# Optimization experiments

Hardware: AMD Instinct MI355X
Metric: run time of the kernel (lower is better)

The kernel has to match this reference:

```python
import jax, jax.numpy as jnp
import numpy as np

B, N, H, NH, M = 4, 8192, 1024, 16, 64
D = H // NH  # head_dim = 64
SCALE = D ** -0.5


def setup_inputs() -> dict:
    key = jax.random.key(0)
    ks = jax.random.split(key, 10)
    inp = {
        'x': jax.random.normal(ks[0], (B, N, H), jnp.float32),
        'c': jax.random.normal(ks[1], (B, H), jnp.float32),
        'w_kv': jax.random.normal(ks[2], (H, 2 * H), jnp.float32) * (H ** -0.5),
        'b_kv': jnp.zeros((2 * H,), jnp.float32),
        'w_temp': jax.random.normal(ks[3], (H, NH), jnp.float32) * (H ** -0.5),
        'b_temp': jnp.zeros((NH,), jnp.float32),
        'xq': jax.random.normal(ks[4], (NH, M, D), jnp.float32) * (D ** -0.5),
        'qkv_proj': jax.random.normal(ks[5], (NH, D, 3 * D), jnp.float32) * 0.02,
        'w_out': jax.random.normal(ks[6], (H, H), jnp.float32) * (H ** -0.5),
        'b_out': jnp.zeros((H,), jnp.float32),
    }
    return inp


def reference(x, c, w_kv, b_kv, w_temp, b_temp, xq, qkv_proj, w_out, b_out):
    b, n, h = x.shape
    # kv slice projections -> [b, h, n, d]
    kv = x @ w_kv + b_kv
    xk, xv = jnp.split(kv, 2, axis=-1)
    xk = xk.reshape(b, n, NH, D).transpose(0, 2, 1, 3)
    xv = xv.reshape(b, n, NH, D).transpose(0, 2, 1, 3)
    # per-token learned temperature: [b, n, heads] -> [b, heads, 1, n]
    temperature = 0.5 + jax.nn.softplus(x @ w_temp + b_temp)
    temperature = temperature.transpose(0, 2, 1)[:, :, None, :]
    # slice scores and softmax over SLICE (query) dim m
    slice_scores = jnp.einsum('hmd,bhnd->bhmn', xq, xk)
    slice_weights = jax.nn.softmax(slice_scores / temperature, axis=-2)
    slice_norm = slice_weights.sum(axis=-1)  # [b, h, m]
    slice_token = jnp.einsum('bhmn,bhnd->bhmd', slice_weights, xv)
    slice_token = slice_token / (slice_norm[..., None] + 1e-5)
    # tiny intra-slice 'attention' (faithfully elementwise, softmax over d)
    qkv = jnp.einsum('bhmd,hde->bhme', slice_token, qkv_proj)
    q_t, k_t, v_t = jnp.split(qkv, 3, axis=-1)
    dots = q_t * k_t * SCALE          # einsum 'bhqd,bhdq->bhqd' == elementwise
    attn = jax.nn.softmax(dots, axis=-1)
    out_slice_token = attn * v_t       # einsum 'bhqd,bhqd->bhqd' == elementwise
    # scatter back to tokens via slice_weights
    out_x = jnp.einsum('bhmd,bhmn->bhnd', out_slice_token, slice_weights)
    out_x = out_x.transpose(0, 2, 1, 3).reshape(b, n, h)
    return out_x @ w_out + b_out
```

## Files before the change

kernel.cpp:

```cpp
#include <hip/hip_runtime.h>
#include <hip/hip_bf16.h>


#define NTOK 32768
#define HH   1024
#define NHD  16
#define DD   64

typedef short short8 __attribute__((ext_vector_type(8)));
typedef float f32x4 __attribute__((ext_vector_type(4)));

#define AS1 __attribute__((address_space(1)))
#define AS3 __attribute__((address_space(3)))

__device__ __forceinline__ void glds16(const void* g, void* l) {
  __builtin_amdgcn_global_load_lds((const AS1 void*)g, (AS3 void*)l, 16, 0, 0);
}

__device__ __forceinline__ void split1(float v, __hip_bfloat16& h, __hip_bfloat16& l) {
  h = __float2bfloat16(v);
  l = __float2bfloat16(v - __bfloat162float(h));
}


__global__ __launch_bounds__(256) void k_acat_t(const float* __restrict__ w_kv,
                                                const float* __restrict__ xq,
                                                __hip_bfloat16* __restrict__ wbth,
                                                __hip_bfloat16* __restrict__ wbtl) {
  int hd = blockIdx.x >> 3, kt = blockIdx.x & 7, k0 = kt * 128;
  __shared__ float xqs[64 * 65];
  __shared__ float wks[128 * 65];
  int t = threadIdx.x;
  for (int j = 0; j < 16; ++j) {
    int idx = t + 256 * j; int m = idx >> 6, d = idx & 63;
    xqs[m * 65 + d] = xq[hd * 4096 + idx];
  }
  for (int j = 0; j < 32; ++j) {
    int idx = t + 256 * j; int r = idx >> 6, c = idx & 63;
    wks[r * 65 + c] = w_kv[(size_t)(k0 + r) * 2048 + hd * 64 + c];
  }
  __syncthreads();
  int m = t & 63, kg = t >> 6;
  __hip_bfloat16 hbuf[32], lbuf[32];
  for (int i = 0; i < 32; ++i) {
    int k = kg * 32 + i;
    float s = 0.f;
    #pragma unroll 8
    for (int d = 0; d < 64; ++d) s = fmaf(wks[k * 65 + d], xqs[m * 65 + d], s);
    split1(s, hbuf[i], lbuf[i]);
  }
  size_t o = (size_t)(hd * 64 + m) * 1024 + k0 + kg * 32;
  for (int i = 0; i < 32; i += 8) {
    *(uint4*)&wbth[o + i] = *(uint4*)&hbuf[i];
    *(uint4*)&wbtl[o + i] = *(uint4*)&lbuf[i];
  }
}

__global__ __launch_bounds__(256) void k_tsplit(const float* __restrict__ src, int ld,
                                                __hip_bfloat16* __restrict__ dh,
                                                __hip_bfloat16* __restrict__ dl) {
  __shared__ float tile[64 * 65];
  int br = blockIdx.y * 64, bc = blockIdx.x * 64;
  int t = threadIdx.x;
  for (int j = 0; j < 16; ++j) {
    int idx = t + 256 * j; int r = idx >> 6, c = idx & 63;
    tile[r * 65 + c] = src[(size_t)(br + r) * ld + bc + c];
  }
  __syncthreads();
  for (int j = 0; j < 16; ++j) {
    int idx = t + 256 * j; int c = idx >> 6, r = idx & 63;
    float v = tile[r * 65 + c];
    __hip_bfloat16 hv, lv; split1(v, hv, lv);
    size_t o = (size_t)(bc + c) * 1024 + br + r;
    dh[o] = hv; dl[o] = lv;
  }
}

__global__ void k_split(const float* __restrict__ src, __hip_bfloat16* __restrict__ hi,
                        __hip_bfloat16* __restrict__ lo) {
  size_t base = ((size_t)blockIdx.x * 256 + threadIdx.x) * 8;
  float4 v0 = *(const float4*)&src[base];
  float4 v1 = *(const float4*)&src[base + 4];
  float vv[8] = {v0.x, v0.y, v0.z, v0.w, v1.x, v1.y, v1.z, v1.w};
  __hip_bfloat16 h8[8], l8[8];
  #pragma unroll
  for (int i = 0; i < 8; ++i) split1(vv[i], h8[i], l8[i]);
  *(uint4*)&hi[base] = *(uint4*)h8;
  *(uint4*)&lo[base] = *(uint4*)l8;
}

__global__ __launch_bounds__(512, 2) void k_mfma8(
    const __hip_bfloat16* __restrict__ Ah, const __hip_bfloat16* __restrict__ Al,
    const __hip_bfloat16* __restrict__ Bh, const __hip_bfloat16* __restrict__ Bl,
    const float* __restrict__ bias, float* __restrict__ C, int ldc) {
  __shared__ __align__(16) char lds[131072];
  const int t = threadIdx.x;
  const int w = t >> 6, lane = t & 63;

  const int gx = gridDim.x;
  const int nwg = gx * gridDim.y;
  const int bid = blockIdx.y * gx + blockIdx.x;
  const int swzb = (bid & 7) * (nwg >> 3) + (bid >> 3);
  const int n0 = (swzb % gx) * 256;
  const int m0 = (swzb / gx) * 256;

  const int wr = w >> 2, wc = w & 3;
  const int fm = lane & 15, kq = lane >> 4;

  int offA[8], offB[4];
  #pragma unroll
  for (int i = 0; i < 8; ++i) {
    int row = wr * 128 + i * 16 + fm;
    offA[i] = (row >> 1) * 128 + ((((row & 1) << 2) | kq) ^ ((row >> 1) & 7)) * 16;
  }
  #pragma unroll
  for (int j = 0; j < 4; ++j) {
    int row = wc * 64 + j * 16 + fm;
    offB[j] = (row >> 1) * 128 + ((((row & 1) << 2) | kq) ^ ((row >> 1) & 7)) * 16;
  }

  const int sp = lane >> 3, su = (lane & 7) ^ sp;
  const int srow = 2 * sp + (su >> 2);
  const int scol = (su & 3) * 8;
  const int aO0 = (m0 + w * 16 + srow) * 1024 + scol;
  const int aO1 = aO0 + 128 * 1024;
  const int bO0 = (n0 + w * 16 + srow) * 1024 + scol;
  const int bO1 = bO0 + 128 * 1024;
  const int ldst = w * 1024 + lane * 16;

  f32x4 acc[8][4];
  #pragma unroll
  for (int i = 0; i < 8; ++i)
    #pragma unroll
    for (int j = 0; j < 4; ++j) acc[i][j] = (f32x4){0.f, 0.f, 0.f, 0.f};

  auto stage = [&](int ts) {
    int koff = (ts >> 1) * 32;
    char* buf = &lds[(ts & 3) * 32768];
    const __hip_bfloat16* As = (ts & 1) ? Al : Ah;
    const __hip_bfloat16* Bs = (ts & 1) ? Bl : Bh;
    glds16(As + aO0 + koff, buf + ldst);
    glds16(As + aO1 + koff, buf + 8192 + ldst);
    glds16(Bs + bO0 + koff, buf + 16384 + ldst);
    glds16(Bs + bO1 + koff, buf + 24576 + ldst);
  };

  stage(0); stage(1); stage(2);
  asm volatile("s_waitcnt vmcnt(8)" ::: "memory");
  __builtin_amdgcn_s_barrier();
  __builtin_amdgcn_sched_barrier(0);

  short8 ah[8], bh[4], xb[4];
  for (int k = 0; k < 32; ++k) {
    const int v0 = 2 * k, v1 = v0 + 1;
    const char* rb0 = &lds[(v0 & 3) * 32768];
    const char* rb1 = &lds[(v1 & 3) * 32768];

    int ts0 = v0 + 3; if (ts0 > 63) ts0 = 63;
    stage(ts0);
    #pragma unroll
    for (int i = 0; i < 8; ++i) ah[i] = *(const short8*)(rb0 + offA[i]);
    #pragma unroll
    for (int j = 0; j < 4; ++j) bh[j] = *(const short8*)(rb0 + 16384 + offB[j]);
    __builtin_amdgcn_s_setprio(1);
    #pragma unroll
    for (int i = 0; i < 8; ++i)
      #pragma unroll
      for (int j = 0; j < 4; ++j)
        acc[i][j] = __builtin_amdgcn_mfma_f32_16x16x32_bf16(ah[i], bh[j], acc[i][j], 0, 0, 0);
    __builtin_amdgcn_s_setprio(0);
    asm volatile("s_waitcnt vmcnt(8)" ::: "memory");
    __builtin_amdgcn_s_barrier();
    __builtin_amdgcn_sched_barrier(0);

    int ts1 = v1 + 3; if (ts1 > 63) ts1 = 63;
    stage(ts1);
    #pragma unroll
    for (int j = 0; j < 4; ++j) xb[j] = *(const short8*)(rb1 + 16384 + offB[j]);
    __builtin_amdgcn_s_setprio(1);
    #pragma unroll
    for (int i = 0; i < 8; ++i)
      #pragma unroll
      for (int j = 0; j < 4; ++j)
        acc[i][j] = __builtin_amdgcn_mfma_f32_16x16x32_bf16(ah[i], xb[j], acc[i][j], 0, 0, 0);
    __builtin_amdgcn_s_setprio(0);
    #pragma unroll
    for (int i = 0; i < 8; ++i) ah[i] = *(const short8*)(rb1 + offA[i]);
    __builtin_amdgcn_s_setprio(1);
    #pragma unroll
    for (int i = 0; i < 8; ++i)
      #pragma unroll
      for (int j = 0; j < 4; ++j)
        acc[i][j] = __builtin_amdgcn_mfma_f32_16x16x32_bf16(ah[i], bh[j], acc[i][j], 0, 0, 0);
    __builtin_amdgcn_s_setprio(0);
    asm volatile("s_waitcnt vmcnt(8)" ::: "memory");
    __builtin_amdgcn_s_barrier();
    __builtin_amdgcn_sched_barrier(0);
  }

  asm volatile("s_waitcnt vmcnt(0)" ::: "memory");
  __builtin_amdgcn_sched_barrier(0);

  const int cm = (lane >> 4) * 4, cn = lane & 15;
  #pragma unroll
  for (int j = 0; j < 4; ++j) {
    int col = n0 + wc * 64 + j * 16 + cn;
    float bbv = bias[col];
    #pragma unroll
    for (int i = 0; i < 8; ++i) {
      int row = m0 + wr * 128 + i * 16 + cm;
      f32x4 v = acc[i][j];
      #pragma unroll
      for (int r = 0; r < 4; ++r)
        C[(size_t)(row + r) * ldc + col] = v[r] + bbv;
    }
  }
}

__global__ __launch_bounds__(256) void k_acat(const float* __restrict__ w_kv,
                                              const float* __restrict__ xq,
                                              float* __restrict__ wbig) {
  int h = blockIdx.x >> 3, kt = blockIdx.x & 7, k0 = kt * 128;
  __shared__ float xqs[64 * 68];
  __shared__ float wks[128 * 68];
  int t = threadIdx.x;
  for (int j = 0; j < 16; ++j) {
    int idx = t + 256 * j; int m = idx >> 6, d = idx & 63;
    xqs[m * 68 + d] = xq[h * 4096 + idx];
  }
  for (int j = 0; j < 32; ++j) {
    int idx = t + 256 * j; int r = idx >> 6, c = idx & 63;
    wks[r * 68 + c] = w_kv[(k0 + r) * 2048 + h * 64 + c];
  }
  __syncthreads();
  int k = t >> 1, half = t & 1;
  float out[32];
  for (int mi = 0; mi < 32; ++mi) {
    int m = half * 32 + mi;
    float s = 0.f;
    #pragma unroll 8
    for (int d = 0; d < 64; ++d) s = fmaf(wks[k * 68 + d], xqs[m * 68 + d], s);
    out[mi] = s;
  }
  float* dst = &wbig[(k0 + k) * 2048 + h * 64 + half * 32];
  for (int mi = 0; mi < 32; mi += 4)
    *(float4*)(dst + mi) = make_float4(out[mi], out[mi + 1], out[mi + 2], out[mi + 3]);
}

__global__ void k_copyv(const float* __restrict__ w_kv, float* __restrict__ wbig) {
  int idx4 = blockIdx.x * 256 + threadIdx.x;
  int k = idx4 >> 8, j4 = idx4 & 255;
  int off = k * 2048 + 1024 + j4 * 4;
  *(float4*)(wbig + off) = *(const float4*)(w_kv + off);
}

__global__ void k_bias1(const float* __restrict__ xq, const float* __restrict__ b_kv,
                        float* __restrict__ bias1) {
  int j = blockIdx.x * 256 + threadIdx.x;
  if (j < 1024) {
    int h = j >> 6, m = j & 63;
    float s = 0.f;
    for (int d = 0; d < 64; ++d) s = fmaf(xq[h * 4096 + m * 64 + d], b_kv[h * 64 + d], s);
    bias1[j] = s;
  } else {
    bias1[j] = b_kv[j];
  }
}

__global__ __launch_bounds__(256) void k_temp(const float* __restrict__ x,
                                              const float* __restrict__ w_temp,
                                              const float* __restrict__ b_temp,
                                              float* __restrict__ T) {
  __shared__ float xs[16 * 1028];
  int t = threadIdx.x;
  int bn0 = blockIdx.x * 16;
  for (int j = 0; j < 16; ++j) {
    int idx4 = t + 256 * j; int row = idx4 >> 8, c4 = (idx4 & 255) * 4;
    *(float4*)&xs[row * 1028 + c4] = *(const float4*)&x[(bn0 + row) * 1024 + c4];
  }
  __syncthreads();
  int tok = t >> 4, j = t & 15;
  float z = b_temp[j];
  for (int k = 0; k < 1024; ++k) z = fmaf(xs[tok * 1028 + k], w_temp[k * 16 + j], z);
  float sp = fmaxf(z, 0.f) + log1pf(expf(-fabsf(z)));
  T[(bn0 + tok) * 16 + j] = 0.5f + sp;
}

__global__ __launch_bounds__(256) void k_gemm(const float* __restrict__ A, int lda,
                                              const float* __restrict__ Bm, int ldb,
                                              const float* __restrict__ bias,
                                              float* __restrict__ C, int ldc, int K) {
  __shared__ float As[8 * 132];
  __shared__ float Bs[8 * 132];
  int t = threadIdx.x;
  int m0 = blockIdx.y * 128, n0 = blockIdx.x * 128;
  int ar = t >> 1, ac = (t & 1) * 4;
  int bk = t >> 5, bc = (t & 31) * 4;
  const float* Ag = A + (size_t)(m0 + ar) * lda + ac;
  const float* Bg = Bm + (size_t)bk * ldb + n0 + bc;
  int tx = t & 15, ty = t >> 4;
  float acc[8][8] = {};
  float4 a4 = *(const float4*)Ag;
  float4 b4 = *(const float4*)Bg;
  for (int kt = 0; kt < K; kt += 8) {
    __syncthreads();
    As[(ac + 0) * 132 + ar] = a4.x;
    As[(ac + 1) * 132 + ar] = a4.y;
    As[(ac + 2) * 132 + ar] = a4.z;
    As[(ac + 3) * 132 + ar] = a4.w;
    *(float4*)&Bs[bk * 132 + bc] = b4;
    __syncthreads();
    if (kt + 8 < K) {
      a4 = *(const float4*)(Ag + kt + 8);
      b4 = *(const float4*)(Bg + (size_t)(kt + 8) * ldb);
    }
    #pragma unroll
    for (int k = 0; k < 8; ++k) {
      float av[8], bv[8];
      *(float4*)&av[0] = *(float4*)&As[k * 132 + ty * 8];
      *(float4*)&av[4] = *(float4*)&As[k * 132 + ty * 8 + 4];
      *(float4*)&bv[0] = *(float4*)&Bs[k * 132 + tx * 4];
      *(float4*)&bv[4] = *(float4*)&Bs[k * 132 + 64 + tx * 4];
      #pragma unroll
      for (int i = 0; i < 8; ++i)
        #pragma unroll
        for (int j = 0; j < 8; ++j) acc[i][j] = fmaf(av[i], bv[j], acc[i][j]);
    }
  }
  float4 bb0 = *(const float4*)&bias[n0 + tx * 4];
  float4 bb1 = *(const float4*)&bias[n0 + 64 + tx * 4];
  #pragma unroll
  for (int i = 0; i < 8; ++i) {
    float* crow = C + (size_t)(m0 + ty * 8 + i) * ldc + n0;
    float4 o0 = make_float4(acc[i][0] + bb0.x, acc[i][1] + bb0.y,
                            acc[i][2] + bb0.z, acc[i][3] + bb0.w);
    float4 o1 = make_float4(acc[i][4] + bb1.x, acc[i][5] + bb1.y,
                            acc[i][6] + bb1.z, acc[i][7] + bb1.w);
    *(float4*)&crow[tx * 4] = o0;
    *(float4*)&crow[64 + tx * 4] = o1;
  }
}

__global__ __launch_bounds__(256) void k_smax(float* __restrict__ S, const float* __restrict__ T,
                                              float* __restrict__ token, float* __restrict__ norm) {
  int pair = blockIdx.x >> 3, chunk = blockIdx.x & 7;
  int b = pair >> 4, h = pair & 15;
  __shared__ float sm[128 * 68];
  __shared__ float xv[128 * 68];
  int t = threadIdx.x;
  int m = t >> 2, dg = t & 3;
  float acc[16] = {};
  float nacc = 0.f;
  for (int s = 0; s < 8; ++s) {
    int bn0 = b * 8192 + chunk * 1024 + s * 128;
    for (int jj = 0; jj < 8; ++jj) {
      int idx4 = t + 256 * jj; int row = idx4 >> 4, c4 = (idx4 & 15) * 4;
      int g = (bn0 + row) * 2048 + h * 64 + c4;
      *(float4*)&sm[row * 68 + c4] = *(const float4*)&S[g];
      *(float4*)&xv[row * 68 + c4] = *(const float4*)&S[g + 1024];
    }
    __syncthreads();
    if (t < 128) {
      float tt = T[(bn0 + t) * 16 + h];
      float inv = 1.f / tt;
      float* row = &sm[t * 68];
      float mx = -1e30f;
      for (int mm = 0; mm < 64; ++mm) mx = fmaxf(mx, row[mm]);
      float sum = 0.f;
      for (int mm = 0; mm < 64; ++mm) { float e = expf((row[mm] - mx) * inv); row[mm] = e; sum += e; }
      float sinv = 1.f / sum;
      for (int mm = 0; mm < 64; ++mm) row[mm] *= sinv;
    }
    __syncthreads();
    for (int jj = 0; jj < 8; ++jj) {
      int idx4 = t + 256 * jj; int row = idx4 >> 4, c4 = (idx4 & 15) * 4;
      int g = (bn0 + row) * 2048 + h * 64 + c4;
      *(float4*)&S[g] = *(const float4*)&sm[row * 68 + c4];
    }
    for (int n = 0; n < 128; ++n) {
      float w = sm[n * 68 + m];
      if (dg == 0) nacc += w;
      const float* xr = &xv[n * 68 + dg * 16];
      #pragma unroll
      for (int q = 0; q < 4; ++q) {
        float4 v = *(const float4*)&xr[q * 4];
        acc[q * 4 + 0] = fmaf(w, v.x, acc[q * 4 + 0]);
        acc[q * 4 + 1] = fmaf(w, v.y, acc[q * 4 + 1]);
        acc[q * 4 + 2] = fmaf(w, v.z, acc[q * 4 + 2]);
        acc[q * 4 + 3] = fmaf(w, v.w, acc[q * 4 + 3]);
      }
    }
    __syncthreads();
  }
  int tb = pair * 4096 + m * 64 + dg * 16;
  for (int q = 0; q < 16; ++q) atomicAdd(&token[tb + q], acc[q]);
  if (dg == 0) atomicAdd(&norm[pair * 64 + m], nacc);
}

__global__ __launch_bounds__(256) void k_stagec(const float* __restrict__ token,
                                                const float* __restrict__ norm,
                                                const float* __restrict__ proj,
                                                float* __restrict__ ost) {
  int pair = blockIdx.x; int h = pair & 15;
  __shared__ float st[64 * 68];
  __shared__ float qk[64 * 196];
  int t = threadIdx.x;
  for (int j = 0; j < 16; ++j) {
    int idx = t + 256 * j; int m = idx >> 6, d = idx & 63;
    st[m * 68 + d] = token[pair * 4096 + idx] / (norm[pair * 64 + m] + 1e-5f);
  }
  __syncthreads();
  for (int idx = t; idx < 64 * 192; idx += 256) {
    int m = idx / 192, e = idx % 192;
    float s = 0.f;
    const float* pr = &proj[h * 12288 + e];
    const float* sr = &st[m * 68];
    for (int d = 0; d < 64; ++d) s = fmaf(sr[d], pr[d * 192], s);
    qk[m * 196 + e] = s;
  }
  __syncthreads();
  if (t < 64) {
    const float* q = &qk[t * 196];
    float dots[64];
    float mx = -1e30f;
    for (int d = 0; d < 64; ++d) { dots[d] = q[d] * q[64 + d] * 0.125f; mx = fmaxf(mx, dots[d]); }
    float sum = 0.f;
    for (int d = 0; d < 64; ++d) { dots[d] = expf(dots[d] - mx); sum += dots[d]; }
    float sinv = 1.f / sum;
    for (int d = 0; d < 64; ++d) ost[pair * 4096 + t * 64 + d] = dots[d] * sinv * q[128 + d];
  }
}

__global__ __launch_bounds__(256) void k_staged(float* __restrict__ S, const float* __restrict__ ost) {
  int pair = blockIdx.x >> 6, chunk = blockIdx.x & 63;
  int b = pair >> 4, h = pair & 15;
  __shared__ float ws[128 * 68];
  int t = threadIdx.x;
  int bn0 = b * 8192 + chunk * 128;
  for (int jj = 0; jj < 8; ++jj) {
    int idx4 = t + 256 * jj; int row = idx4 >> 4, c4 = (idx4 & 15) * 4;
    *(float4*)&ws[row * 68 + c4] = *(const float4*)&S[(bn0 + row) * 2048 + h * 64 + c4];
  }
  int d = t & 63, ng = t >> 6;
  float o[64];
  #pragma unroll
  for (int mm = 0; mm < 64; ++mm) o[mm] = ost[pair * 4096 + mm * 64 + d];
  __syncthreads();
  for (int i = 0; i < 32; ++i) {
    int n = ng + 4 * i;
    const float* wr = &ws[n * 68];
    float s = 0.f;
    #pragma unroll
    for (int mm = 0; mm < 64; ++mm) s = fmaf(wr[mm], o[mm], s);
    S[(bn0 + n) * 2048 + 1024 + h * 64 + d] = s;
  }
}

__global__ __launch_bounds__(256) void k_staged_bf(const float* __restrict__ S,
                                                   const float* __restrict__ ost,
                                                   __hip_bfloat16* __restrict__ oxh,
                                                   __hip_bfloat16* __restrict__ oxl) {
  int pair = blockIdx.x >> 6, chunk = blockIdx.x & 63;
  int b = pair >> 4, hd = pair & 15;
  __shared__ float ws[128 * 68];
  int t = threadIdx.x;
  int bn0 = b * 8192 + chunk * 128;
  for (int jj = 0; jj < 8; ++jj) {
    int idx4 = t + 256 * jj; int row = idx4 >> 4, c4 = (idx4 & 15) * 4;
    *(float4*)&ws[row * 68 + c4] = *(const float4*)&S[(bn0 + row) * 2048 + hd * 64 + c4];
  }
  int d = t & 63, ng = t >> 6;
  float o[64];
  #pragma unroll
  for (int mm = 0; mm < 64; ++mm) o[mm] = ost[pair * 4096 + mm * 64 + d];
  __syncthreads();
  for (int i = 0; i < 32; ++i) {
    int n = ng + 4 * i;
    const float* wr = &ws[n * 68];
    float s = 0.f;
    #pragma unroll
    for (int mm = 0; mm < 64; ++mm) s = fmaf(wr[mm], o[mm], s);
    __hip_bfloat16 hv, lv; split1(s, hv, lv);
    size_t oo = (size_t)(bn0 + n) * 1024 + hd * 64 + d;
    oxh[oo] = hv; oxl[oo] = lv;
  }
}

extern "C" void kernel_launch(void* const* d_in, const int* in_sizes, int n_in,
                              void* d_out, int out_size, void* d_ws, size_t ws_size,
                              hipStream_t stream) {
  const float* x      = (const float*)d_in[0];
  const float* w_kv   = (const float*)d_in[2];
  const float* b_kv   = (const float*)d_in[3];
  const float* w_temp = (const float*)d_in[4];
  const float* b_temp = (const float*)d_in[5];
  const float* xq     = (const float*)d_in[6];
  const float* proj   = (const float*)d_in[7];
  const float* w_out  = (const float*)d_in[8];
  const float* b_out  = (const float*)d_in[9];
  float* out = (float*)d_out;

  float* ws    = (float*)d_ws;
  float* S     = ws;
  float* T     = S + 67108864;
  float* BIAS1 = T + 524288;
  float* TOKEN = BIAS1 + 2048;
  float* NORM  = TOKEN + 262144;
  float* OST   = NORM + 4096;
  float* FEND  = OST + 262144;
  __hip_bfloat16* WbTh = (__hip_bfloat16*)FEND;
  __hip_bfloat16* WbTl = WbTh + 2097152;
  __hip_bfloat16* WoTh = WbTl + 2097152;
  __hip_bfloat16* WoTl = WoTh + 1048576;
  __hip_bfloat16* XH   = WoTl + 1048576;
  __hip_bfloat16* XL   = XH + 33554432;
  const size_t need_fast = 419454976ULL;

  hipMemsetAsync(TOKEN, 0, (262144 + 4096) * sizeof(float), stream);
  k_bias1<<<8, 256, 0, stream>>>(xq, b_kv, BIAS1);
  k_temp<<<2048, 256, 0, stream>>>(x, w_temp, b_temp, T);

  if (ws_size >= need_fast) {
    k_acat_t<<<128, 256, 0, stream>>>(w_kv, xq, WbTh, WbTl);
    k_tsplit<<<dim3(16, 16), 256, 0, stream>>>(w_kv + 1024, 2048,
                                               WbTh + 1048576, WbTl + 1048576);
    k_tsplit<<<dim3(16, 16), 256, 0, stream>>>(w_out, 1024, WoTh, WoTl);
    k_split<<<16384, 256, 0, stream>>>(x, XH, XL);
    k_mfma8<<<dim3(8, 128), 512, 0, stream>>>(XH, XL, WbTh, WbTl, BIAS1, S, 2048);
    k_smax<<<512, 256, 0, stream>>>(S, T, TOKEN, NORM);
    k_stagec<<<64, 256, 0, stream>>>(TOKEN, NORM, proj, OST);
    k_staged_bf<<<4096, 256, 0, stream>>>(S, OST, XH, XL);
    k_mfma8<<<dim3(4, 128), 512, 0, stream>>>(XH, XL, WoTh, WoTl, b_out, out, 1024);
  } else {
    float* WBIG = (float*)WbTh;
    k_acat<<<128, 256, 0, stream>>>(w_kv, xq, WBIG);
    k_copyv<<<1024, 256, 0, stream>>>(w_kv, WBIG);
    k_gemm<<<dim3(16, 256), 256, 0, stream>>>(x, 1024, WBIG, 2048, BIAS1, S, 2048, 1024);
    k_smax<<<512, 256, 0, stream>>>(S, T, TOKEN, NORM);
    k_stagec<<<64, 256, 0, stream>>>(TOKEN, NORM, proj, OST);
    k_staged<<<4096, 256, 0, stream>>>(S, OST);
    k_gemm<<<dim3(8, 256), 256, 0, stream>>>(S + 1024, 2048, w_out, 1024, b_out, out, 1024, 1024);
  }
}
```

Measured before the change: 1.417 ms.

## Register-tile slice accumulation, vectorize scatter-back, reorder LDS reads before staging

Rewrites the softmax/slice-token accumulation so each thread holds a 4x16 register tile over token subsets, reads weights as vectors, and reduces the four warp partials through LDS before the atomics. This lowers LDS traffic per FMA and cuts the number of global atomics. The scatter-back kernel now computes two output columns per thread with vectorized LDS reads and writes packed bf16 pairs. In the GEMM main loop, the LDS fragment reads are moved ahead of the async global-to-LDS staging call. The cost is higher register pressure and an extra LDS reduction pass.

```diff
diff --git a/kernel.cpp b/kernel.cpp
--- a/kernel.cpp
+++ b/kernel.cpp
@@ -157,11 +157,11 @@
     const char* rb1 = &lds[(v1 & 3) * 32768];
 
     int ts0 = v0 + 3; if (ts0 > 63) ts0 = 63;
+    #pragma unroll
+    for (int j = 0; j < 4; ++j) bh[j] = *(const short8*)(rb0 + 16384 + offB[j]);
+    #pragma unroll
+    for (int i = 0; i < 8; ++i) ah[i] = *(const short8*)(rb0 + offA[i]);
     stage(ts0);
-    #pragma unroll
-    for (int i = 0; i < 8; ++i) ah[i] = *(const short8*)(rb0 + offA[i]);
-    #pragma unroll
-    for (int j = 0; j < 4; ++j) bh[j] = *(const short8*)(rb0 + 16384 + offB[j]);
     __builtin_amdgcn_s_setprio(1);
     #pragma unroll
     for (int i = 0; i < 8; ++i)
@@ -174,9 +174,9 @@
     __builtin_amdgcn_sched_barrier(0);
 
     int ts1 = v1 + 3; if (ts1 > 63) ts1 = 63;
+    #pragma unroll
+    for (int j = 0; j < 4; ++j) xb[j] = *(const short8*)(rb1 + 16384 + offB[j]);
     stage(ts1);
-    #pragma unroll
-    for (int j = 0; j < 4; ++j) xb[j] = *(const short8*)(rb1 + 16384 + offB[j]);
     __builtin_amdgcn_s_setprio(1);
     #pragma unroll
     for (int i = 0; i < 8; ++i)
@@ -345,12 +345,19 @@
                                               float* __restrict__ token, float* __restrict__ norm) {
   int pair = blockIdx.x >> 3, chunk = blockIdx.x & 7;
   int b = pair >> 4, h = pair & 15;
-  __shared__ float sm[128 * 68];
-  __shared__ float xv[128 * 68];
-  int t = threadIdx.x;
-  int m = t >> 2, dg = t & 3;
-  float acc[16] = {};
-  float nacc = 0.f;
+  __shared__ float lsh[17408];
+  float* sm = lsh;
+  float* xv = lsh + 8704;
+  int t = threadIdx.x;
+  int lane = t & 63, ng = t >> 6;
+  int mb = (lane & 15) * 4;
+  int db = (lane >> 4) * 16;
+  f32x4 acc4[4][4];
+  #pragma unroll
+  for (int i = 0; i < 4; ++i)
+    #pragma unroll
+    for (int q = 0; q < 4; ++q) acc4[i][q] = (f32x4){0.f, 0.f, 0.f, 0.f};
+  float nacc[4] = {0.f, 0.f, 0.f, 0.f};
   for (int s = 0; s < 8; ++s) {
     int bn0 = b * 8192 + chunk * 1024 + s * 128;
     for (int jj = 0; jj < 8; ++jj) {
@@ -377,24 +384,53 @@
       int g = (bn0 + row) * 2048 + h * 64 + c4;
       *(float4*)&S[g] = *(const float4*)&sm[row * 68 + c4];
     }
-    for (int n = 0; n < 128; ++n) {
-      float w = sm[n * 68 + m];
-      if (dg == 0) nacc += w;
-      const float* xr = &xv[n * 68 + dg * 16];
+    for (int i = 0; i < 32; ++i) {
+      int n = ng * 32 + i;
+      f32x4 w4 = *(const f32x4*)&sm[n * 68 + mb];
+      f32x4 x0 = *(const f32x4*)&xv[n * 68 + db];
+      f32x4 x1 = *(const f32x4*)&xv[n * 68 + db + 4];
+      f32x4 x2 = *(const f32x4*)&xv[n * 68 + db + 8];
+      f32x4 x3 = *(const f32x4*)&xv[n * 68 + db + 12];
+      if ((lane >> 4) == 0) {
+        nacc[0] += w4[0]; nacc[1] += w4[1]; nacc[2] += w4[2]; nacc[3] += w4[3];
+      }
       #pragma unroll
-      for (int q = 0; q < 4; ++q) {
-        float4 v = *(const float4*)&xr[q * 4];
-        acc[q * 4 + 0] = fmaf(w, v.x, acc[q * 4 + 0]);
-        acc[q * 4 + 1] = fmaf(w, v.y, acc[q * 4 + 1]);
-        acc[q * 4 + 2] = fmaf(w, v.z, acc[q * 4 + 2]);
-        acc[q * 4 + 3] = fmaf(w, v.w, acc[q * 4 + 3]);
+      for (int mi = 0; mi < 4; ++mi) {
+        float wm = w4[mi];
+        f32x4 wv = (f32x4){wm, wm, wm, wm};
+        acc4[mi][0] += wv * x0;
+        acc4[mi][1] += wv * x1;
+        acc4[mi][2] += wv * x2;
+        acc4[mi][3] += wv * x3;
       }
     }
     __syncthreads();
   }
-  int tb = pair * 4096 + m * 64 + dg * 16;
-  for (int q = 0; q < 16; ++q) atomicAdd(&token[tb + q], acc[q]);
-  if (dg == 0) atomicAdd(&norm[pair * 64 + m], nacc);
+  float* red = lsh;
+  #pragma unroll
+  for (int mi = 0; mi < 4; ++mi)
+    #pragma unroll
+    for (int q = 0; q < 4; ++q)
+      *(f32x4*)&red[ng * 4096 + (mb + mi) * 64 + db + q * 4] = acc4[mi][q];
+  __syncthreads();
+  int c0 = t * 16;
+  for (int j4 = 0; j4 < 4; ++j4) {
+    int c = c0 + j4 * 4;
+    f32x4 r0 = *(const f32x4*)&red[c];
+    f32x4 r1 = *(const f32x4*)&red[4096 + c];
+    f32x4 r2 = *(const f32x4*)&red[8192 + c];
+    f32x4 r3 = *(const f32x4*)&red[12288 + c];
+    f32x4 sum = (r0 + r1) + (r2 + r3);
+    atomicAdd(&token[pair * 4096 + c + 0], sum[0]);
+    atomicAdd(&token[pair * 4096 + c + 1], sum[1]);
+    atomicAdd(&token[pair * 4096 + c + 2], sum[2]);
+    atomicAdd(&token[pair * 4096 + c + 3], sum[3]);
+  }
+  if (lane < 16) {
+    #pragma unroll
+    for (int mi = 0; mi < 4; ++mi)
+      atomicAdd(&norm[pair * 64 + mb + mi], nacc[mi]);
+  }
 }
 
 __global__ __launch_bounds__(256) void k_stagec(const float* __restrict__ token,
@@ -464,25 +500,35 @@
   int b = pair >> 4, hd = pair & 15;
   __shared__ float ws[128 * 68];
   int t = threadIdx.x;
+  int d2 = t & 31, ng = t >> 5;
   int bn0 = b * 8192 + chunk * 128;
   for (int jj = 0; jj < 8; ++jj) {
     int idx4 = t + 256 * jj; int row = idx4 >> 4, c4 = (idx4 & 15) * 4;
     *(float4*)&ws[row * 68 + c4] = *(const float4*)&S[(bn0 + row) * 2048 + hd * 64 + c4];
   }
-  int d = t & 63, ng = t >> 6;
-  float o[64];
-  #pragma unroll
-  for (int mm = 0; mm < 64; ++mm) o[mm] = ost[pair * 4096 + mm * 64 + d];
-  __syncthreads();
-  for (int i = 0; i < 32; ++i) {
-    int n = ng + 4 * i;
-    const float* wr = &ws[n * 68];
-    float s = 0.f;
-    #pragma unroll
-    for (int mm = 0; mm < 64; ++mm) s = fmaf(wr[mm], o[mm], s);
-    __hip_bfloat16 hv, lv; split1(s, hv, lv);
-    size_t oo = (size_t)(bn0 + n) * 1024 + hd * 64 + d;
-    oxh[oo] = hv; oxl[oo] = lv;
+  float2 o2[64];
+  #pragma unroll
+  for (int mm = 0; mm < 64; ++mm)
+    o2[mm] = *(const float2*)&ost[pair * 4096 + mm * 64 + 2 * d2];
+  __syncthreads();
+  for (int i = 0; i < 16; ++i) {
+    int n = ng * 16 + i;
+    float a0 = 0.f, a1 = 0.f;
+    #pragma unroll
+    for (int mq = 0; mq < 16; ++mq) {
+      f32x4 wv = *(const f32x4*)&ws[n * 68 + mq * 4];
+      a0 = fmaf(wv[0], o2[mq * 4 + 0].x, a0); a1 = fmaf(wv[0], o2[mq * 4 + 0].y, a1);
+      a0 = fmaf(wv[1], o2[mq * 4 + 1].x, a0); a1 = fmaf(wv[1], o2[mq * 4 + 1].y, a1);
+      a0 = fmaf(wv[2], o2[mq * 4 + 2].x, a0); a1 = fmaf(wv[2], o2[mq * 4 + 2].y, a1);
+      a0 = fmaf(wv[3], o2[mq * 4 + 3].x, a0); a1 = fmaf(wv[3], o2[mq * 4 + 3].y, a1);
+    }
+    __hip_bfloat16 hb[2] __attribute__((aligned(4)));
+    __hip_bfloat16 lb[2] __attribute__((aligned(4)));
+    split1(a0, hb[0], lb[0]);
+    split1(a1, hb[1], lb[1]);
+    size_t oo = (size_t)(bn0 + n) * 1024 + hd * 64 + 2 * d2;
+    *(uint*)&oxh[oo] = *(const uint*)hb;
+    *(uint*)&oxl[oo] = *(const uint*)lb;
   }
 }
 
```

New measurement: 1.342 ms. 1.06x faster.
